# Kernel optimization log

Measured on AMD Instinct MI355X. Metric: run time of the kernel, lower is better.

Reference implementation:

```python
import jax, jax.numpy as jnp
import numpy as np

N, F_IN, F_OUT, C = 4096, 512, 256, 4


def setup_inputs() -> dict:
    key = jax.random.key(0)
    k1, k2, k3, k4 = jax.random.split(key, 4)
    stdv = 1.0 / np.sqrt(F_OUT)
    x = jax.random.normal(k1, (N, F_IN), dtype=jnp.float32)
    adjs = jax.random.normal(k2, (N, N, C), dtype=jnp.float32)
    weight = jax.random.uniform(k3, (F_IN, F_OUT, C), dtype=jnp.float32, minval=-stdv, maxval=stdv)
    bias = jax.random.uniform(k4, (N, F_OUT, C), dtype=jnp.float32, minval=-stdv, maxval=stdv)
    return {"x": x, "adjs": adjs, "weight": weight, "bias": bias}


def _fft_product(X, Y):
    # t-product: FFT along channel axis, per-frequency matmul, IFFT, real part
    Xf = jnp.fft.fft(X, axis=-1)
    Yf = jnp.fft.fft(Y, axis=-1)
    Zf = jnp.einsum('ijk,jrk->irk', Xf, Yf)
    return jnp.fft.ifft(Zf, axis=-1).real.astype(X.dtype)


def reference(x, adjs, weight, bias):
    C_ = adjs.shape[-1]
    # x.repeat(C,1,1).permute(1,2,0) -> [N, F, C]
    x3 = jnp.broadcast_to(x[:, :, None], (x.shape[0], x.shape[1], C_))
    h = _fft_product(x3, weight)      # [N, F_OUT, C]
    out = _fft_product(adjs, h)       # [N, F_OUT, C]
    return out + bias
```

## Files before the change

kernel.cpp:

```cpp
#include <hip/hip_runtime.h>
#include <cstdint>
#include <cstddef>

#define NN   4096
#define FIN  512
#define FOUT 256

typedef short bf16x8 __attribute__((ext_vector_type(8)));
typedef float f32x4  __attribute__((ext_vector_type(4)));
typedef float f32x2  __attribute__((ext_vector_type(2)));

__device__ __forceinline__ unsigned short f2bf(float f) {
    union { float f; unsigned u; } v; v.f = f;
    unsigned r = v.u + 0x7FFFu + ((v.u >> 16) & 1u);
    return (unsigned short)(r >> 16);
}
__device__ __forceinline__ unsigned pack2(float a, float b) {
    return (unsigned)f2bf(a) | ((unsigned)f2bf(b) << 16);
}

__global__ __launch_bounds__(256) void k_prep_wsum(const f32x4* __restrict__ w4,
                                                   unsigned short* __restrict__ wsumT) {
    int t = blockIdx.x * 256 + threadIdx.x;
    int r = t & (FOUT - 1);
    int j = t >> 8;
    f32x4 v = w4[j * FOUT + r];
    wsumT[r * FIN + j] = f2bf((v.x + v.y) + (v.z + v.w));
}

__global__ __launch_bounds__(512) void k_gemm_h(const float* __restrict__ x,
                                                const unsigned short* __restrict__ Bt,
                                                unsigned short* __restrict__ Ht) {
    __shared__ unsigned short Abf[16 * 72];
    const int tid  = threadIdx.x;
    const int lane = tid & 63;
    const int wave = tid >> 6;
    const int quad = lane >> 4;
    const int l15  = lane & 15;
    const int i0   = blockIdx.x * 16;
    const int si   = tid >> 5;
    const int sk   = (tid & 31) * 2;

    f32x4 acc0 = {0.f, 0.f, 0.f, 0.f};
    f32x4 acc1 = {0.f, 0.f, 0.f, 0.f};

    f32x2 pf;
    bf16x8 bp00, bp01, bp10, bp11;

    auto loadA = [&](int c) {
        pf = *(const f32x2*)(x + (size_t)(i0 + si) * FIN + c * 64 + sk);
    };
    auto loadB = [&](int c, bf16x8& b00, bf16x8& b01, bf16x8& b10, bf16x8& b11) {
        const unsigned short* p0 = Bt + (size_t)(wave * 32 + l15) * FIN + c * 64 + quad * 8;
        b00 = *(const bf16x8*)(p0);
        b01 = *(const bf16x8*)(p0 + 32);
        const unsigned short* p1 = p0 + (size_t)16 * FIN;
        b10 = *(const bf16x8*)(p1);
        b11 = *(const bf16x8*)(p1 + 32);
    };

    loadA(0);
    loadB(0, bp00, bp01, bp10, bp11);

    for (int c = 0; c < FIN / 64; ++c) {
        __syncthreads();
        *(unsigned*)&Abf[si * 72 + sk] = pack2(pf.x, pf.y);
        __syncthreads();

        bf16x8 bc00 = bp00, bc01 = bp01, bc10 = bp10, bc11 = bp11;
        if (c + 1 < FIN / 64) {
            loadA(c + 1);
            loadB(c + 1, bp00, bp01, bp10, bp11);
        }
        bf16x8 a0 = *(const bf16x8*)&Abf[l15 * 72 + quad * 8];
        bf16x8 a1 = *(const bf16x8*)&Abf[l15 * 72 + 32 + quad * 8];

        acc0 = __builtin_amdgcn_mfma_f32_16x16x32_bf16(a0, bc00, acc0, 0, 0, 0);
        acc0 = __builtin_amdgcn_mfma_f32_16x16x32_bf16(a1, bc01, acc0, 0, 0, 0);
        acc1 = __builtin_amdgcn_mfma_f32_16x16x32_bf16(a0, bc10, acc1, 0, 0, 0);
        acc1 = __builtin_amdgcn_mfma_f32_16x16x32_bf16(a1, bc11, acc1, 0, 0, 0);
    }

    const int n  = wave * 32 + l15;
    const int ib = i0 + quad * 4;
    ushort4 h;
    h.x = f2bf(acc0[0]); h.y = f2bf(acc0[1]); h.z = f2bf(acc0[2]); h.w = f2bf(acc0[3]);
    *(ushort4*)(Ht + (size_t)n * NN + ib) = h;
    h.x = f2bf(acc1[0]); h.y = f2bf(acc1[1]); h.z = f2bf(acc1[2]); h.w = f2bf(acc1[3]);
    *(ushort4*)(Ht + (size_t)(n + 16) * NN + ib) = h;
}

#define LD 72
__global__ __launch_bounds__(512) void k_gemm_big(const f32x4* __restrict__ adjs4,
                                                  const unsigned short* __restrict__ Bt,
                                                  float* __restrict__ P) {
    __shared__ unsigned short Abf[2][64 * LD];

    const int tid  = threadIdx.x;
    const int lane = tid & 63;
    const int wave = tid >> 6;
    const int quad = lane >> 4;
    const int l15  = lane & 15;

    const int kq   = blockIdx.x & 3;
    const int rg   = blockIdx.x >> 2;
    const int row0 = rg * 64;
    const size_t kbase = (size_t)kq * 1024;

    const int sr = tid >> 3;
    const int sc = tid & 7;

    f32x4 acc[4][2];
#pragma unroll
    for (int m = 0; m < 4; ++m)
#pragma unroll
        for (int n = 0; n < 2; ++n)
            acc[m][n] = (f32x4){0.f, 0.f, 0.f, 0.f};

    f32x4 pa[8];
    bf16x8 pb[2][2];

    auto loadA = [&](int c) {
        const f32x4* ap = adjs4 + (size_t)(row0 + sr) * NN + kbase + c * 64;
#pragma unroll
        for (int u = 0; u < 4; ++u) {
            pa[2 * u]     = __builtin_nontemporal_load(ap + sc * 2 + u * 16);
            pa[2 * u + 1] = __builtin_nontemporal_load(ap + sc * 2 + u * 16 + 1);
        }
    };
    auto writeA = [&](int b) {
        unsigned* dst = (unsigned*)&Abf[b][sr * LD + sc * 2];
#pragma unroll
        for (int u = 0; u < 4; ++u) {
            f32x4 p0 = pa[2 * u], p1 = pa[2 * u + 1];
            dst[u * 8] = pack2((p0.x + p0.y) + (p0.z + p0.w),
                               (p1.x + p1.y) + (p1.z + p1.w));
        }
    };
    auto loadB = [&](int c) {
#pragma unroll
        for (int n = 0; n < 2; ++n) {
            const unsigned short* p = Bt + (size_t)(wave * 32 + n * 16 + l15) * NN
                                        + kbase + c * 64 + quad * 8;
            pb[n][0] = *(const bf16x8*)p;
            pb[n][1] = *(const bf16x8*)(p + 32);
        }
    };

    loadA(0);
    loadB(0);

    for (int c = 0; c < 16; ++c) {
        const int b = c & 1;
        writeA(b);
        if (c + 1 < 16) loadA(c + 1);
        __syncthreads();

        bf16x8 bc[2][2] = {{pb[0][0], pb[0][1]}, {pb[1][0], pb[1][1]}};
        if (c + 1 < 16) loadB(c + 1);

#pragma unroll
        for (int s = 0; s < 2; ++s) {
#pragma unroll
            for (int m = 0; m < 4; ++m) {
                bf16x8 a = *(const bf16x8*)&Abf[b][(m * 16 + l15) * LD + s * 32 + quad * 8];
                acc[m][0] = __builtin_amdgcn_mfma_f32_16x16x32_bf16(a, bc[0][s], acc[m][0], 0, 0, 0);
                acc[m][1] = __builtin_amdgcn_mfma_f32_16x16x32_bf16(a, bc[1][s], acc[m][1], 0, 0, 0);
            }
        }
        __syncthreads();
    }

    float* p = P + (size_t)kq * NN * FOUT;
#pragma unroll
    for (int m = 0; m < 4; ++m) {
#pragma unroll
        for (int n = 0; n < 2; ++n) {
            const int col = wave * 32 + n * 16 + l15;
#pragma unroll
            for (int r = 0; r < 4; ++r) {
                const int row = row0 + m * 16 + quad * 4 + r;
                p[(size_t)row * FOUT + col] = acc[m][n][r];
            }
        }
    }
}

__global__ __launch_bounds__(256) void k_reduce(const float* __restrict__ P,
                                                const f32x4* __restrict__ bias4,
                                                f32x4* __restrict__ out4) {
    const int idx = blockIdx.x * 256 + threadIdx.x;
    const size_t STR = (size_t)NN * FOUT;
    float s = (P[idx] + P[idx + STR]) + (P[idx + 2 * STR] + P[idx + 3 * STR]);
    f32x4 bv = bias4[idx];
    f32x4 o;
    o.x = s + bv.x; o.y = s + bv.y; o.z = s + bv.z; o.w = s + bv.w;
    out4[idx] = o;
}

extern "C" void kernel_launch(void* const* d_in, const int* in_sizes, int n_in,
                              void* d_out, int out_size, void* d_ws, size_t ws_size,
                              hipStream_t stream) {
    const float* x     = (const float*)d_in[0];
    const f32x4* adjs4 = (const f32x4*)d_in[1];
    const f32x4* w4    = (const f32x4*)d_in[2];
    const f32x4* bias4 = (const f32x4*)d_in[3];
    f32x4*       out4  = (f32x4*)d_out;

    char* ws = (char*)d_ws;
    unsigned short* wsumT = (unsigned short*)ws;
    unsigned short* Ht    = (unsigned short*)(ws + 262144);
    float*          Pp    = (float*)(ws + 262144 + 2097152);

    k_prep_wsum<<<(FIN * FOUT) / 256, 256, 0, stream>>>(w4, wsumT);
    k_gemm_h<<<NN / 16, 512, 0, stream>>>(x, wsumT, Ht);
    k_gemm_big<<<256, 512, 0, stream>>>(adjs4, Ht, Pp);
    k_reduce<<<(NN * FOUT) / 256, 256, 0, stream>>>(Pp, bias4, out4);
}
```

Baseline: 395.7 us.

## Halve big GEMM row tile, double grid, deepen adjs prefetch, use lightweight barriers

```diff
diff --git a/kernel.cpp b/kernel.cpp
--- a/kernel.cpp
+++ b/kernel.cpp
@@ -9,6 +9,10 @@
 typedef short bf16x8 __attribute__((ext_vector_type(8)));
 typedef float f32x4  __attribute__((ext_vector_type(4)));
 typedef float f32x2  __attribute__((ext_vector_type(2)));
+
+#define BAR() do { asm volatile("s_waitcnt lgkmcnt(0)" ::: "memory"); \
+                   __builtin_amdgcn_s_barrier();                      \
+                   asm volatile("" ::: "memory"); } while (0)
 
 __device__ __forceinline__ unsigned short f2bf(float f) {
     union { float f; unsigned u; } v; v.f = f;
@@ -63,9 +67,9 @@
     loadB(0, bp00, bp01, bp10, bp11);
 
     for (int c = 0; c < FIN / 64; ++c) {
-        __syncthreads();
+        BAR();
         *(unsigned*)&Abf[si * 72 + sk] = pack2(pf.x, pf.y);
-        __syncthreads();
+        BAR();
 
         bf16x8 bc00 = bp00, bc01 = bp01, bc10 = bp10, bc11 = bp11;
         if (c + 1 < FIN / 64) {
@@ -91,10 +95,10 @@
 }
 
 #define LD 72
-__global__ __launch_bounds__(512) void k_gemm_big(const f32x4* __restrict__ adjs4,
-                                                  const unsigned short* __restrict__ Bt,
-                                                  float* __restrict__ P) {
-    __shared__ unsigned short Abf[2][64 * LD];
+__global__ __launch_bounds__(512, 4) void k_gemm_big(const f32x4* __restrict__ adjs4,
+                                                     const unsigned short* __restrict__ Bt,
+                                                     float* __restrict__ P) {
+    __shared__ unsigned short Abf[2][32 * LD];
 
     const int tid  = threadIdx.x;
     const int lane = tid & 63;
@@ -104,37 +108,39 @@
 
     const int kq   = blockIdx.x & 3;
     const int rg   = blockIdx.x >> 2;
-    const int row0 = rg * 64;
+    const int row0 = rg * 32;
     const size_t kbase = (size_t)kq * 1024;
 
-    const int sr = tid >> 3;
-    const int sc = tid & 7;
-
-    f32x4 acc[4][2];
-#pragma unroll
-    for (int m = 0; m < 4; ++m)
+    const int sr = tid >> 4;
+    const int sc = tid & 15;
+
+    f32x4 acc[2][2];
+#pragma unroll
+    for (int m = 0; m < 2; ++m)
 #pragma unroll
         for (int n = 0; n < 2; ++n)
             acc[m][n] = (f32x4){0.f, 0.f, 0.f, 0.f};
 
-    f32x4 pa[8];
+    f32x4 pa[2][4];
     bf16x8 pb[2][2];
 
     auto loadA = [&](int c) {
         const f32x4* ap = adjs4 + (size_t)(row0 + sr) * NN + kbase + c * 64;
-#pragma unroll
-        for (int u = 0; u < 4; ++u) {
-            pa[2 * u]     = __builtin_nontemporal_load(ap + sc * 2 + u * 16);
-            pa[2 * u + 1] = __builtin_nontemporal_load(ap + sc * 2 + u * 16 + 1);
-        }
-    };
-    auto writeA = [&](int b) {
+        f32x4* d = pa[c & 1];
+#pragma unroll
+        for (int v = 0; v < 2; ++v) {
+            d[2 * v]     = __builtin_nontemporal_load(ap + sc * 2 + v * 32);
+            d[2 * v + 1] = __builtin_nontemporal_load(ap + sc * 2 + v * 32 + 1);
+        }
+    };
+    auto writeA = [&](int b, int c) {
+        const f32x4* s = pa[c & 1];
         unsigned* dst = (unsigned*)&Abf[b][sr * LD + sc * 2];
 #pragma unroll
-        for (int u = 0; u < 4; ++u) {
-            f32x4 p0 = pa[2 * u], p1 = pa[2 * u + 1];
-            dst[u * 8] = pack2((p0.x + p0.y) + (p0.z + p0.w),
-                               (p1.x + p1.y) + (p1.z + p1.w));
+        for (int v = 0; v < 2; ++v) {
+            f32x4 p0 = s[2 * v], p1 = s[2 * v + 1];
+            dst[v * 16] = pack2((p0.x + p0.y) + (p0.z + p0.w),
+                                (p1.x + p1.y) + (p1.z + p1.w));
         }
     };
     auto loadB = [&](int c) {
@@ -149,31 +155,33 @@
 
     loadA(0);
     loadB(0);
+    writeA(0, 0);
+    loadA(1);
+    BAR();
 
     for (int c = 0; c < 16; ++c) {
         const int b = c & 1;
-        writeA(b);
-        if (c + 1 < 16) loadA(c + 1);
-        __syncthreads();
-
+        if (c + 2 < 16) loadA(c + 2);
         bf16x8 bc[2][2] = {{pb[0][0], pb[0][1]}, {pb[1][0], pb[1][1]}};
-        if (c + 1 < 16) loadB(c + 1);
-
+        if (c + 1 < 16) {
+            writeA(b ^ 1, c + 1);
+            loadB(c + 1);
+        }
 #pragma unroll
         for (int s = 0; s < 2; ++s) {
 #pragma unroll
-            for (int m = 0; m < 4; ++m) {
+            for (int m = 0; m < 2; ++m) {
                 bf16x8 a = *(const bf16x8*)&Abf[b][(m * 16 + l15) * LD + s * 32 + quad * 8];
                 acc[m][0] = __builtin_amdgcn_mfma_f32_16x16x32_bf16(a, bc[0][s], acc[m][0], 0, 0, 0);
                 acc[m][1] = __builtin_amdgcn_mfma_f32_16x16x32_bf16(a, bc[1][s], acc[m][1], 0, 0, 0);
             }
         }
-        __syncthreads();
+        BAR();
     }
 
     float* p = P + (size_t)kq * NN * FOUT;
 #pragma unroll
-    for (int m = 0; m < 4; ++m) {
+    for (int m = 0; m < 2; ++m) {
 #pragma unroll
         for (int n = 0; n < 2; ++n) {
             const int col = wave * 32 + n * 16 + l15;
@@ -214,6 +222,6 @@
 
     k_prep_wsum<<<(FIN * FOUT) / 256, 256, 0, stream>>>(w4, wsumT);
     k_gemm_h<<<NN / 16, 512, 0, stream>>>(x, wsumT, Ht);
-    k_gemm_big<<<256, 512, 0, stream>>>(adjs4, Ht, Pp);
+    k_gemm_big<<<512, 512, 0, stream>>>(adjs4, Ht, Pp);
     k_reduce<<<(NN * FOUT) / 256, 256, 0, stream>>>(Pp, bias4, out4);
 }
```

Result: slower. 409.7 us (+3.5%).
